# Kernel optimization log

Measured on AMD Instinct MI355X. Metric: run time of the kernel, lower is better.

The kernel has to match this reference:

```python
import jax, jax.numpy as jnp
import numpy as np

NUM_SEGMENTS = 4096  # number of graphs in the batch


def setup_inputs() -> dict:
    key = jax.random.key(0)
    k1, k2, k3, k4, k5, k6 = jax.random.split(key, 6)
    N, H = 1048576, 128
    x = jax.random.normal(k1, (N, H), dtype=jnp.float32)
    batch = jnp.sort(jax.random.randint(k2, (N,), 0, NUM_SEGMENTS, dtype=jnp.int64))
    # Linear params, PyTorch layout: W [out, in], b [out]
    W1 = jax.random.normal(k3, (2 * H, H), dtype=jnp.float32) * (1.0 / np.sqrt(H))
    b1 = jax.random.normal(k4, (2 * H,), dtype=jnp.float32) * 0.01
    W2 = jax.random.normal(k5, (H, 2 * H), dtype=jnp.float32) * (1.0 / np.sqrt(2 * H))
    b2 = jax.random.normal(k6, (H,), dtype=jnp.float32) * 0.01
    return {"x": x, "batch": batch, "W1": W1, "b1": b1, "W2": W2, "b2": b2}


def reference(x, batch, W1, b1, W2, b2):
    # phi(x) = tanh(fc1(x))  -> [N, 2H]
    phi_x = jnp.tanh(jnp.einsum('nh,oh->no', x, W1) + b1)
    # scatter-sum pooling per graph -> [G, 2H]
    sum_x = jax.ops.segment_sum(phi_x, batch, num_segments=NUM_SEGMENTS)
    # fc2 -> [G, H]; .squeeze() is a no-op for these shapes
    y = jnp.einsum('go,ho->gh', sum_x, W2) + b2
    return jnp.squeeze(y)
```

## Files before the change

### kernel.cpp

```cpp
#include <hip/hip_runtime.h>
#include <hip/hip_bf16.h>

#define NTOT 1048576
#define NSEG 4096
#define HDIM 128
#define ODIM 256
#define BN   64

typedef __attribute__((ext_vector_type(8))) short bf16x8;
typedef __attribute__((ext_vector_type(4))) float f32x4;
typedef __attribute__((ext_vector_type(2))) unsigned int u32x2;

__device__ __forceinline__ unsigned short f32_to_bf16_rne(float f) {
    unsigned int u = __builtin_bit_cast(unsigned int, f);
    unsigned int r = (u + 0x7fffu + ((u >> 16) & 1u)) >> 16;
    return (unsigned short)r;
}
__device__ __forceinline__ unsigned int pk_bf16(float lo, float hi) {
    return ((unsigned int)f32_to_bf16_rne(hi) << 16) | f32_to_bf16_rne(lo);
}

__global__ void convert_w1(const float* __restrict__ W1, unsigned int* __restrict__ W1b) {
    int i = blockIdx.x * 256 + threadIdx.x;
    float2 v = *(const float2*)(W1 + 2 * i);
    W1b[i] = pk_bf16(v.x, v.y);
}

__global__ __launch_bounds__(256, 4)
void stage1(const float* __restrict__ x, const int* __restrict__ batch,
            const unsigned short* __restrict__ W1b, const float* __restrict__ b1,
            float* __restrict__ sumx) {
    __shared__ __align__(16) unsigned char smem[BN * 256];
    __shared__ int seg[BN];

    const int t    = threadIdx.x;
    const int lane = t & 63;
    const int wv   = t >> 6;
    const int l15  = lane & 15;
    const int lhi  = lane >> 4;
    const long n0  = (long)blockIdx.x * BN;

    const bool is64 = (batch[NTOT - 1] == 0);
    if (t < BN) {
        long idx = n0 + t;
        seg[t] = batch[is64 ? 2 * idx : idx];
    }

    #pragma unroll
    for (int i = 0; i < 8; ++i) {
        int idx = i * 256 + t;
        int row = idx >> 5;
        int c4  = idx & 31;
        const float4 xv = *(const float4*)(x + (n0 + row) * HDIM + c4 * 4);
        u32x2 p;
        p.x = pk_bf16(xv.x, xv.y);
        p.y = pk_bf16(xv.z, xv.w);
        int boff = row * 256 + ((c4 * 8) ^ ((row & 7) << 4));
        *(u32x2*)(smem + boff) = p;
    }
    __syncthreads();

    f32x4 acc[4][4];
    #pragma unroll
    for (int nf = 0; nf < 4; ++nf) {
        float bb = b1[wv * 64 + nf * 16 + l15];
        #pragma unroll
        for (int mf = 0; mf < 4; ++mf)
            acc[mf][nf] = (f32x4){bb, bb, bb, bb};
    }

    #pragma unroll
    for (int ks = 0; ks < 4; ++ks) {
        const int k0 = ks * 32 + lhi * 8;
        bf16x8 bfrag[4];
        #pragma unroll
        for (int nf = 0; nf < 4; ++nf) {
            int n = wv * 64 + nf * 16 + l15;
            bfrag[nf] = *(const bf16x8*)(W1b + n * HDIM + k0);
        }
        bf16x8 afrag[4];
        #pragma unroll
        for (int mf = 0; mf < 4; ++mf) {
            int m = mf * 16 + l15;
            int boff = m * 256 + ((k0 * 2) ^ ((m & 7) << 4));
            afrag[mf] = *(const bf16x8*)(smem + boff);
        }
        #pragma unroll
        for (int mf = 0; mf < 4; ++mf)
            #pragma unroll
            for (int nf = 0; nf < 4; ++nf)
                acc[mf][nf] = __builtin_amdgcn_mfma_f32_16x16x32_bf16(
                    afrag[mf], bfrag[nf], acc[mf][nf], 0, 0, 0);
    }

    #pragma unroll
    for (int mf = 0; mf < 4; ++mf)
        #pragma unroll
        for (int nf = 0; nf < 4; ++nf)
            #pragma unroll
            for (int r = 0; r < 4; ++r) {
                float e = exp2f(acc[mf][nf][r] * 2.885390081777927f);
                acc[mf][nf][r] = 1.0f - 2.0f * __builtin_amdgcn_rcpf(1.0f + e);
            }

    unsigned long long bmask;
    {
        int s_here = seg[lane];
        int s_prev = (lane > 0) ? seg[lane - 1] : s_here;
        bmask = __ballot(s_here != s_prev);
    }

    int start = 0;
    unsigned long long rem = bmask;
    for (;;) {
        const int end = rem ? (int)__builtin_ctzll(rem) : BN;
        const int sid = seg[start];
        float p0 = 0.f, p1 = 0.f, p2 = 0.f, p3 = 0.f;
        #pragma unroll
        for (int mf = 0; mf < 4; ++mf)
            #pragma unroll
            for (int r = 0; r < 4; ++r) {
                int row = mf * 16 + lhi * 4 + r;
                float w = ((unsigned)(row - start) < (unsigned)(end - start)) ? 1.0f : 0.0f;
                p0 = fmaf(w, acc[mf][0][r], p0);
                p1 = fmaf(w, acc[mf][1][r], p1);
                p2 = fmaf(w, acc[mf][2][r], p2);
                p3 = fmaf(w, acc[mf][3][r], p3);
            }
        p0 += __shfl_xor(p0, 16); p0 += __shfl_xor(p0, 32);
        p1 += __shfl_xor(p1, 16); p1 += __shfl_xor(p1, 32);
        p2 += __shfl_xor(p2, 16); p2 += __shfl_xor(p2, 32);
        p3 += __shfl_xor(p3, 16); p3 += __shfl_xor(p3, 32);
        if (lhi == 0) {
            float* base = sumx + (long)sid * ODIM + wv * 64 + l15;
            atomicAdd(base +  0, p0);
            atomicAdd(base + 16, p1);
            atomicAdd(base + 32, p2);
            atomicAdd(base + 48, p3);
        }
        if (rem == 0) break;
        start = end;
        rem &= rem - 1;
    }
}

__global__ __launch_bounds__(256)
void stage2(const float* __restrict__ sumx, const float* __restrict__ W2,
            const float* __restrict__ b2, float* __restrict__ y) {
    __shared__ float sx[16 * 256];
    const int t = threadIdx.x;
    const long g0 = (long)blockIdx.x * 16;
    #pragma unroll
    for (int i = 0; i < 16; ++i)
        sx[i * 256 + t] = sumx[(g0 + i) * 256 + t];
    __syncthreads();
    const int h = t & 127;
    const int gl0 = (t >> 7) * 8;
    float acc[8] = {0, 0, 0, 0, 0, 0, 0, 0};
    const float* w = W2 + h * 256;
    for (int o4 = 0; o4 < 64; ++o4) {
        float4 wvv = *(const float4*)(w + o4 * 4);
        #pragma unroll
        for (int gl = 0; gl < 8; ++gl) {
            const float* sr = &sx[(gl0 + gl) * 256 + o4 * 4];
            acc[gl] += sr[0] * wvv.x + sr[1] * wvv.y + sr[2] * wvv.z + sr[3] * wvv.w;
        }
    }
    float bb = b2[h];
    #pragma unroll
    for (int gl = 0; gl < 8; ++gl)
        y[(g0 + gl0 + gl) * 128 + h] = acc[gl] + bb;
}

extern "C" void kernel_launch(void* const* d_in, const int* in_sizes, int n_in,
                              void* d_out, int out_size, void* d_ws, size_t ws_size,
                              hipStream_t stream) {
    const float* x   = (const float*)d_in[0];
    const int* batch = (const int*)d_in[1];
    const float* W1  = (const float*)d_in[2];
    const float* b1  = (const float*)d_in[3];
    const float* W2  = (const float*)d_in[4];
    const float* b2  = (const float*)d_in[5];
    float* y = (float*)d_out;

    float* sumx = (float*)d_ws;
    unsigned short* W1b = (unsigned short*)((char*)d_ws + (size_t)NSEG * ODIM * 4);

    (void)hipMemsetAsync(sumx, 0, (size_t)NSEG * ODIM * sizeof(float), stream);
    convert_w1<<<dim3((ODIM * HDIM / 2) / 256), dim3(256), 0, stream>>>(W1, (unsigned int*)W1b);
    stage1<<<dim3(NTOT / BN), dim3(256), 0, stream>>>(x, batch, W1b, b1, sumx);
    stage2<<<dim3(NSEG / 16), dim3(256), 0, stream>>>(sumx, W2, b2, y);
}
```

Measured before the change: 234.4 us.

## Make stage1 persistent with double-buffered x tiles and fuse memset into W1 conversion

Stage1 now launches 1024 persistent blocks, each handling 16 consecutive 64-row tiles. The x loads for the next tile are prefetched into registers while the current tile runs its MFMA, tanh and segment atomics, then written into a second shared-memory buffer, which hides global-load latency. The separate memset of sumx is folded into the W1 bf16 conversion kernel, saving one launch. In exchange, register pressure rises from the 8 held float4 prefetches, shared memory doubles, and the grid is smaller, which may reduce occupancy.

New measurement: 494.9 us. 2.11x slower.

```diff
diff --git a/kernel.cpp b/kernel.cpp
--- a/kernel.cpp
+++ b/kernel.cpp
@@ -6,6 +6,8 @@
 #define HDIM 128
 #define ODIM 256
 #define BN   64
+#define GRID1 1024
+#define TPB  (NTOT / (BN * GRID1))
 
 typedef __attribute__((ext_vector_type(8))) short bf16x8;
 typedef __attribute__((ext_vector_type(4))) float f32x4;
@@ -20,127 +22,170 @@
     return ((unsigned int)f32_to_bf16_rne(hi) << 16) | f32_to_bf16_rne(lo);
 }
 
-__global__ void convert_w1(const float* __restrict__ W1, unsigned int* __restrict__ W1b) {
-    int i = blockIdx.x * 256 + threadIdx.x;
-    float2 v = *(const float2*)(W1 + 2 * i);
-    W1b[i] = pk_bf16(v.x, v.y);
+__global__ void zero_convert(const float* __restrict__ W1, unsigned int* __restrict__ W1b,
+                             float* __restrict__ sumx) {
+    int gid = blockIdx.x * 256 + threadIdx.x;
+    sumx[gid] = 0.0f;
+    if (gid < (ODIM * HDIM / 2)) {
+        float2 v = *(const float2*)(W1 + 2 * gid);
+        W1b[gid] = pk_bf16(v.x, v.y);
+    }
 }
 
 __global__ __launch_bounds__(256, 4)
 void stage1(const float* __restrict__ x, const int* __restrict__ batch,
             const unsigned short* __restrict__ W1b, const float* __restrict__ b1,
             float* __restrict__ sumx) {
-    __shared__ __align__(16) unsigned char smem[BN * 256];
-    __shared__ int seg[BN];
+    __shared__ __align__(16) unsigned char smem[2][BN * 256];
+    __shared__ int seg[2][BN];
 
     const int t    = threadIdx.x;
     const int lane = t & 63;
     const int wv   = t >> 6;
     const int l15  = lane & 15;
     const int lhi  = lane >> 4;
-    const long n0  = (long)blockIdx.x * BN;
 
     const bool is64 = (batch[NTOT - 1] == 0);
-    if (t < BN) {
-        long idx = n0 + t;
-        seg[t] = batch[is64 ? 2 * idx : idx];
-    }
-
+    const long tile0 = (long)blockIdx.x * TPB;
+
+    float bias[4];
     #pragma unroll
-    for (int i = 0; i < 8; ++i) {
-        int idx = i * 256 + t;
-        int row = idx >> 5;
-        int c4  = idx & 31;
-        const float4 xv = *(const float4*)(x + (n0 + row) * HDIM + c4 * 4);
-        u32x2 p;
-        p.x = pk_bf16(xv.x, xv.y);
-        p.y = pk_bf16(xv.z, xv.w);
-        int boff = row * 256 + ((c4 * 8) ^ ((row & 7) << 4));
-        *(u32x2*)(smem + boff) = p;
-    }
-    __syncthreads();
-
-    f32x4 acc[4][4];
-    #pragma unroll
-    for (int nf = 0; nf < 4; ++nf) {
-        float bb = b1[wv * 64 + nf * 16 + l15];
+    for (int nf = 0; nf < 4; ++nf) bias[nf] = b1[wv * 64 + nf * 16 + l15];
+
+    {
+        const long n0 = tile0 * BN;
+        float4 pf[8];
+        #pragma unroll
+        for (int i = 0; i < 8; ++i) {
+            int idx = i * 256 + t; int row = idx >> 5; int c4 = idx & 31;
+            pf[i] = *(const float4*)(x + (n0 + row) * HDIM + c4 * 4);
+        }
+        int sv = 0;
+        if (t < BN) sv = batch[is64 ? 2 * (n0 + t) : (n0 + t)];
+        #pragma unroll
+        for (int i = 0; i < 8; ++i) {
+            int idx = i * 256 + t; int row = idx >> 5; int c4 = idx & 31;
+            u32x2 p; p.x = pk_bf16(pf[i].x, pf[i].y); p.y = pk_bf16(pf[i].z, pf[i].w);
+            int boff = row * 256 + ((c4 * 8) ^ ((row & 7) << 4));
+            *(u32x2*)(&smem[0][0] + boff) = p;
+        }
+        if (t < BN) seg[0][t] = sv;
+        __syncthreads();
+    }
+
+    int cur = 0;
+    for (int g = 0; g < TPB; ++g) {
+        const bool more = (g + 1 < TPB);
+
+        float4 pf[8];
+        int sv = 0;
+        if (more) {
+            const long n1 = (tile0 + g + 1) * BN;
+            #pragma unroll
+            for (int i = 0; i < 8; ++i) {
+                int idx = i * 256 + t; int row = idx >> 5; int c4 = idx & 31;
+                pf[i] = *(const float4*)(x + (n1 + row) * HDIM + c4 * 4);
+            }
+            if (t < BN) sv = batch[is64 ? 2 * (n1 + t) : (n1 + t)];
+        }
+
+        const unsigned char* Abuf = &smem[cur][0];
+        const int* segc = &seg[cur][0];
+
+        f32x4 acc[4][4];
+        #pragma unroll
+        for (int nf = 0; nf < 4; ++nf) {
+            float bb = bias[nf];
+            #pragma unroll
+            for (int mf = 0; mf < 4; ++mf)
+                acc[mf][nf] = (f32x4){bb, bb, bb, bb};
+        }
+        #pragma unroll
+        for (int ks = 0; ks < 4; ++ks) {
+            const int k0 = ks * 32 + lhi * 8;
+            bf16x8 bfrag[4];
+            #pragma unroll
+            for (int nf = 0; nf < 4; ++nf) {
+                int n = wv * 64 + nf * 16 + l15;
+                bfrag[nf] = *(const bf16x8*)(W1b + n * HDIM + k0);
+            }
+            bf16x8 afrag[4];
+            #pragma unroll
+            for (int mf = 0; mf < 4; ++mf) {
+                int m = mf * 16 + l15;
+                int boff = m * 256 + ((k0 * 2) ^ ((m & 7) << 4));
+                afrag[mf] = *(const bf16x8*)(Abuf + boff);
+            }
+            #pragma unroll
+            for (int mf = 0; mf < 4; ++mf)
+                #pragma unroll
+                for (int nf = 0; nf < 4; ++nf)
+                    acc[mf][nf] = __builtin_amdgcn_mfma_f32_16x16x32_bf16(
+                        afrag[mf], bfrag[nf], acc[mf][nf], 0, 0, 0);
+        }
+
         #pragma unroll
         for (int mf = 0; mf < 4; ++mf)
-            acc[mf][nf] = (f32x4){bb, bb, bb, bb};
-    }
-
-    #pragma unroll
-    for (int ks = 0; ks < 4; ++ks) {
-        const int k0 = ks * 32 + lhi * 8;
-        bf16x8 bfrag[4];
-        #pragma unroll
-        for (int nf = 0; nf < 4; ++nf) {
-            int n = wv * 64 + nf * 16 + l15;
-            bfrag[nf] = *(const bf16x8*)(W1b + n * HDIM + k0);
-        }
-        bf16x8 afrag[4];
-        #pragma unroll
-        for (int mf = 0; mf < 4; ++mf) {
-            int m = mf * 16 + l15;
-            int boff = m * 256 + ((k0 * 2) ^ ((m & 7) << 4));
-            afrag[mf] = *(const bf16x8*)(smem + boff);
-        }
-        #pragma unroll
-        for (int mf = 0; mf < 4; ++mf)
             #pragma unroll
             for (int nf = 0; nf < 4; ++nf)
-                acc[mf][nf] = __builtin_amdgcn_mfma_f32_16x16x32_bf16(
-                    afrag[mf], bfrag[nf], acc[mf][nf], 0, 0, 0);
-    }
-
-    #pragma unroll
-    for (int mf = 0; mf < 4; ++mf)
-        #pragma unroll
-        for (int nf = 0; nf < 4; ++nf)
-            #pragma unroll
-            for (int r = 0; r < 4; ++r) {
-                float e = exp2f(acc[mf][nf][r] * 2.885390081777927f);
-                acc[mf][nf][r] = 1.0f - 2.0f * __builtin_amdgcn_rcpf(1.0f + e);
-            }
-
-    unsigned long long bmask;
-    {
-        int s_here = seg[lane];
-        int s_prev = (lane > 0) ? seg[lane - 1] : s_here;
-        bmask = __ballot(s_here != s_prev);
-    }
-
-    int start = 0;
-    unsigned long long rem = bmask;
-    for (;;) {
-        const int end = rem ? (int)__builtin_ctzll(rem) : BN;
-        const int sid = seg[start];
-        float p0 = 0.f, p1 = 0.f, p2 = 0.f, p3 = 0.f;
-        #pragma unroll
-        for (int mf = 0; mf < 4; ++mf)
-            #pragma unroll
-            for (int r = 0; r < 4; ++r) {
-                int row = mf * 16 + lhi * 4 + r;
-                float w = ((unsigned)(row - start) < (unsigned)(end - start)) ? 1.0f : 0.0f;
-                p0 = fmaf(w, acc[mf][0][r], p0);
-                p1 = fmaf(w, acc[mf][1][r], p1);
-                p2 = fmaf(w, acc[mf][2][r], p2);
-                p3 = fmaf(w, acc[mf][3][r], p3);
-            }
-        p0 += __shfl_xor(p0, 16); p0 += __shfl_xor(p0, 32);
-        p1 += __shfl_xor(p1, 16); p1 += __shfl_xor(p1, 32);
-        p2 += __shfl_xor(p2, 16); p2 += __shfl_xor(p2, 32);
-        p3 += __shfl_xor(p3, 16); p3 += __shfl_xor(p3, 32);
-        if (lhi == 0) {
-            float* base = sumx + (long)sid * ODIM + wv * 64 + l15;
-            atomicAdd(base +  0, p0);
-            atomicAdd(base + 16, p1);
-            atomicAdd(base + 32, p2);
-            atomicAdd(base + 48, p3);
-        }
-        if (rem == 0) break;
-        start = end;
-        rem &= rem - 1;
+                #pragma unroll
+                for (int r = 0; r < 4; ++r) {
+                    float e = exp2f(acc[mf][nf][r] * 2.885390081777927f);
+                    acc[mf][nf][r] = 1.0f - 2.0f * __builtin_amdgcn_rcpf(1.0f + e);
+                }
+
+        unsigned long long bmask;
+        {
+            int s_here = segc[lane];
+            int s_prev = (lane > 0) ? segc[lane - 1] : s_here;
+            bmask = __ballot(s_here != s_prev);
+        }
+        int start = 0;
+        unsigned long long rem = bmask;
+        for (;;) {
+            const int end = rem ? (int)__builtin_ctzll(rem) : BN;
+            const int sid = segc[start];
+            float p0 = 0.f, p1 = 0.f, p2 = 0.f, p3 = 0.f;
+            #pragma unroll
+            for (int mf = 0; mf < 4; ++mf)
+                #pragma unroll
+                for (int r = 0; r < 4; ++r) {
+                    int row = mf * 16 + lhi * 4 + r;
+                    float w = ((unsigned)(row - start) < (unsigned)(end - start)) ? 1.0f : 0.0f;
+                    p0 = fmaf(w, acc[mf][0][r], p0);
+                    p1 = fmaf(w, acc[mf][1][r], p1);
+                    p2 = fmaf(w, acc[mf][2][r], p2);
+                    p3 = fmaf(w, acc[mf][3][r], p3);
+                }
+            p0 += __shfl_xor(p0, 16); p0 += __shfl_xor(p0, 32);
+            p1 += __shfl_xor(p1, 16); p1 += __shfl_xor(p1, 32);
+            p2 += __shfl_xor(p2, 16); p2 += __shfl_xor(p2, 32);
+            p3 += __shfl_xor(p3, 16); p3 += __shfl_xor(p3, 32);
+            if (lhi == 0) {
+                float* base = sumx + (long)sid * ODIM + wv * 64 + l15;
+                atomicAdd(base +  0, p0);
+                atomicAdd(base + 16, p1);
+                atomicAdd(base + 32, p2);
+                atomicAdd(base + 48, p3);
+            }
+            if (rem == 0) break;
+            start = end;
+            rem &= rem - 1;
+        }
+
+        if (more) {
+            unsigned char* Wbuf = &smem[cur ^ 1][0];
+            #pragma unroll
+            for (int i = 0; i < 8; ++i) {
+                int idx = i * 256 + t; int row = idx >> 5; int c4 = idx & 31;
+                u32x2 p; p.x = pk_bf16(pf[i].x, pf[i].y); p.y = pk_bf16(pf[i].z, pf[i].w);
+                int boff = row * 256 + ((c4 * 8) ^ ((row & 7) << 4));
+                *(u32x2*)(Wbuf + boff) = p;
+            }
+            if (t < BN) seg[cur ^ 1][t] = sv;
+        }
+        __syncthreads();
+        cur ^= 1;
     }
 }
 
@@ -186,8 +231,7 @@
     float* sumx = (float*)d_ws;
     unsigned short* W1b = (unsigned short*)((char*)d_ws + (size_t)NSEG * ODIM * 4);
 
-    (void)hipMemsetAsync(sumx, 0, (size_t)NSEG * ODIM * sizeof(float), stream);
-    convert_w1<<<dim3((ODIM * HDIM / 2) / 256), dim3(256), 0, stream>>>(W1, (unsigned int*)W1b);
-    stage1<<<dim3(NTOT / BN), dim3(256), 0, stream>>>(x, batch, W1b, b1, sumx);
+    zero_convert<<<dim3(NSEG), dim3(256), 0, stream>>>(W1, (unsigned int*)W1b, sumx);
+    stage1<<<dim3(GRID1), dim3(256), 0, stream>>>(x, batch, W1b, b1, sumx);
     stage2<<<dim3(NSEG / 16), dim3(256), 0, stream>>>(sumx, W2, b2, y);
 }
```
